# Kernel optimization log

Measured on AMD Instinct MI355X. Metric: run time of the kernel, lower is better.

The kernel has to match this reference:

```python
import jax, jax.numpy as jnp
import numpy as np

TEMP = 0.1

def _normalized_grid(B, H, W, dtype=jnp.float32):
    # normalized coords in [-1, 1], (x, y) order, shape [B, H, W, 2]
    ys = jnp.linspace(-1.0, 1.0, H, dtype=dtype)
    xs = jnp.linspace(-1.0, 1.0, W, dtype=dtype)
    gy, gx = jnp.meshgrid(ys, xs, indexing='ij')
    grid = jnp.stack([gx, gy], axis=-1)  # [H, W, 2]
    return jnp.broadcast_to(grid, (B, H, W, 2))


def setup_inputs() -> dict:
    key = jax.random.key(0)
    k1, k2, k3 = jax.random.split(key, 3)
    B, H, W, D = 8, 48, 48, 1024
    f_mv_A = jax.random.normal(k1, (B, H, W, D), dtype=jnp.float32)
    f_mv_B = jax.random.normal(k2, (B, H, W, D), dtype=jnp.float32)
    # omega buffer: 2*pi*randn(dim//2, 2)
    omega = 2.0 * jnp.pi * jax.random.normal(k3, (D // 2, 2), dtype=jnp.float32)
    scale = jnp.ones((), dtype=jnp.float32)
    return {"f_mv_A": f_mv_A, "f_mv_B": f_mv_B, "omega": omega, "scale": scale}


def reference(f_mv_A, f_mv_B, omega, scale):
    B, H_A, W_A, D = f_mv_A.shape
    _, H_B, W_B, _ = f_mv_B.shape
    # Fourier positional embedding grid over image B coordinates
    x = _normalized_grid(B, H_B, W_B).reshape(B, H_B * W_B, 2)
    x_emb = x @ (scale * omega).T                      # [B, HW_B, D//2]
    pos_emb_grid = jnp.concatenate([jnp.sin(x_emb), jnp.cos(x_emb)], axis=-1)  # [B, HW_B, D]

    # cosine similarity cross-attention
    fa = f_mv_A / jnp.linalg.norm(f_mv_A, axis=-1, keepdims=True)
    fb = f_mv_B / jnp.linalg.norm(f_mv_B, axis=-1, keepdims=True)
    fa = fa.reshape(B, H_A * W_A, D)
    fb = fb.reshape(B, H_B * W_B, D)
    attn_logits = (1.0 / TEMP) * jnp.einsum('bqd,bkd->bqk', fa, fb)  # [B, HW_A, HW_B]
    attn = jax.nn.softmax(attn_logits, axis=2)
    match_emb = jnp.einsum('bqk,bkd->bqd', attn, pos_emb_grid)        # [B, HW_A, D]

    attn_logits = attn_logits.reshape(B, H_A, W_A, H_B, W_B)
    attn = attn.reshape(B, H_A, W_A, H_B, W_B)
    match_emb = match_emb.reshape(B, H_A, W_A, D)
    return attn_logits, attn, match_emb
```

## Files before the change

kernel.cpp:

```cpp
#include <hip/hip_runtime.h>
#include <stdint.h>
#include <math.h>

#define NBATCH 8
#define HWSZ   2304
#define DDIM   1024
#define NROWS  (NBATCH*HWSZ)
#define PLANE  ((size_t)NROWS*DDIM)
#define OFF1   ((size_t)NBATCH*HWSZ*HWSZ)
#define OFF2   (2*OFF1)

typedef __attribute__((ext_vector_type(8))) short bf16x8;
typedef __attribute__((ext_vector_type(8))) _Float16 f16x8;
typedef __attribute__((ext_vector_type(4))) float f32x4;

__device__ __forceinline__ float bf2f(uint16_t u) {
    union { uint32_t i; float f; } v; v.i = ((uint32_t)u) << 16; return v.f;
}
__device__ __forceinline__ uint16_t f2bf(float f) {
    union { uint32_t i; float f; } v; v.f = f;
    uint32_t x = v.i;
    return (uint16_t)((x + 0x7fffu + ((x >> 16) & 1u)) >> 16);
}
__device__ __forceinline__ float h2f(uint16_t u) {
    _Float16 h; __builtin_memcpy(&h, &u, 2); return (float)h;
}
__device__ __forceinline__ uint16_t f2h(float f) {
    _Float16 h = (_Float16)f; uint16_t u; __builtin_memcpy(&u, &h, 2); return u;
}
__device__ __forceinline__ int dmode(const uint16_t* s) {
    uint16_t v = s[0];
    return (v == 0x3F80u) ? 1 : ((v == 0x3C00u) ? 2 : 0);
}
__device__ __forceinline__ float dec16(uint16_t u, int m) { return (m == 1) ? bf2f(u) : h2f(u); }
__device__ __forceinline__ uint16_t enc16(float f, int m) { return (m == 1) ? f2bf(f) : f2h(f); }

__global__ void layout_probe(int* __restrict__ rowT, int* __restrict__ colT) {
    int lane = threadIdx.x & 63;
    int m = lane & 15, q = lane >> 4;
    bf16x8 a1, b1, a2, b2;
    #pragma unroll
    for (int j = 0; j < 8; j++) {
        int k = q * 8 + j;
        float k0 = (k == 0) ? 1.0f : 0.0f;
        a1[j] = (short)f2bf(k0);
        b1[j] = (short)f2bf(k0 * (float)(m + 1));
        a2[j] = (short)f2bf(k0 * (float)(m + 1));
        b2[j] = (short)f2bf(k0);
    }
    f32x4 z = {0.f, 0.f, 0.f, 0.f};
    f32x4 d1 = __builtin_amdgcn_mfma_f32_16x16x32_bf16(a1, b1, z, 0, 0, 0);
    f32x4 d2 = __builtin_amdgcn_mfma_f32_16x16x32_bf16(a2, b2, z, 0, 0, 0);
    #pragma unroll
    for (int r = 0; r < 4; r++) {
        colT[lane * 4 + r] = (int)d1[r] - 1;
        rowT[lane * 4 + r] = (int)d2[r] - 1;
    }
}

__global__ void rownorm_kernel(const void* __restrict__ inA, const void* __restrict__ inB,
                               const uint16_t* __restrict__ scalep, float* __restrict__ rn,
                               void* __restrict__ outbase) {
    const int mode = dmode(scalep);
    int row = blockIdx.x;
    int t = threadIdx.x;
    const void* src = (row < NROWS) ? inA : inB;
    int lrow = (row < NROWS) ? row : row - NROWS;
    float v[4];
    if (mode == 0) {
        const float* p = (const float*)src + (size_t)lrow * DDIM + t * 4;
        float4 f = *(const float4*)p;
        v[0] = f.x; v[1] = f.y; v[2] = f.z; v[3] = f.w;
        uint16_t* hbase = (uint16_t*)((float*)outbase + OFF1) + ((row < NROWS) ? 0 : PLANE);
        uint16_t h0 = f2h(v[0]), h1 = f2h(v[1]), h2 = f2h(v[2]), h3 = f2h(v[3]);
        uint2 hv;
        hv.x = (uint32_t)h0 | ((uint32_t)h1 << 16);
        hv.y = (uint32_t)h2 | ((uint32_t)h3 << 16);
        *(uint2*)(hbase + (size_t)lrow * DDIM + t * 4) = hv;
    } else {
        const uint16_t* p = (const uint16_t*)src + (size_t)lrow * DDIM + t * 4;
        uint2 u = *(const uint2*)p;
        v[0] = dec16(u.x & 0xffff, mode); v[1] = dec16(u.x >> 16, mode);
        v[2] = dec16(u.y & 0xffff, mode); v[3] = dec16(u.y >> 16, mode);
    }
    float ss = v[0]*v[0] + v[1]*v[1] + v[2]*v[2] + v[3]*v[3];
    __shared__ float red[256];
    red[t] = ss; __syncthreads();
    for (int s = 128; s > 0; s >>= 1) { if (t < s) red[t] += red[t + s]; __syncthreads(); }
    if (t == 0) rn[row] = 1.0f / sqrtf(red[0]);
}

__global__ void posemb_kernel(const void* __restrict__ omega, const uint16_t* __restrict__ scalep,
                              uint16_t* __restrict__ posT) {
    const int mode = dmode(scalep);
    int j = blockIdx.x;
    float om0, om1, sc;
    if (mode == 0) {
        const float* om = (const float*)omega;
        om0 = om[j * 2]; om1 = om[j * 2 + 1];
        sc = *(const float*)scalep;
    } else {
        const uint16_t* om = (const uint16_t*)omega;
        om0 = dec16(om[j * 2], mode); om1 = dec16(om[j * 2 + 1], mode);
        sc = dec16(scalep[0], mode);
    }
    om0 *= sc; om1 *= sc;
    for (int p = threadIdx.x; p < HWSZ; p += 256) {
        int iy = p / 48, ix = p % 48;
        float gx = (2.0f / 47.0f) * (float)ix - 1.0f;
        float gy = (2.0f / 47.0f) * (float)iy - 1.0f;
        float e = om0 * gx + om1 * gy;
        size_t chunk = (size_t)(p >> 5) * (DDIM * 32);
        int kin = p & 31;
        posT[chunk + (size_t)j * 32 + kin]           = f2bf(sinf(e));
        posT[chunk + (size_t)(j + 512) * 32 + kin]   = f2bf(cosf(e));
    }
}

#define LSTR 40

__launch_bounds__(256, 2)
__global__ void gemm1_mfma(const void* __restrict__ inA, const void* __restrict__ inB,
                           const uint16_t* __restrict__ scalep, const float* __restrict__ rn,
                           void* __restrict__ outbase,
                           const int* __restrict__ rowT, const int* __restrict__ colT) {
    const int mode = dmode(scalep);
    __shared__ uint16_t sA[128 * LSTR];
    __shared__ uint16_t sB[128 * LSTR];
    __shared__ float rnS[256];
    int g = blockIdx.x;
    int swz = (g & 7) * 324 + (g >> 3);
    int b = swz / 324;
    int rr = swz % 324;
    int tm = rr / 18, tn = rr % 18;
    int t = threadIdx.x;
    if (t < 128) rnS[t] = 10.0f * rn[(size_t)b * HWSZ + tm * 128 + t];
    else         rnS[t] = rn[(size_t)NROWS + (size_t)b * HWSZ + tn * 128 + (t - 128)];
    int r0c = t >> 2, cb0 = (t & 3) * 8;
    int r1c = r0c + 64;
    int lane = t & 63, wave = t >> 6;
    int wm = (wave & 1) * 64, wn = (wave >> 1) * 64;
    int lr = lane & 15, ko = (lane >> 4) * 8;
    size_t rowA0 = (size_t)b * HWSZ + tm * 128;
    size_t rowB0 = (size_t)b * HWSZ + tn * 128;
    const uint16_t* pA16;
    const uint16_t* pB16;
    if (mode == 0) {
        const uint16_t* planes = (const uint16_t*)((const float*)outbase + OFF1);
        pA16 = planes + rowA0 * DDIM;
        pB16 = planes + PLANE + rowB0 * DDIM;
    } else {
        pA16 = (const uint16_t*)inA + rowA0 * DDIM;
        pB16 = (const uint16_t*)inB + rowB0 * DDIM;
    }
    f32x4 acc[4][4] = {};

    for (int k0 = 0; k0 < DDIM; k0 += 32) {
        uint4 a0 = *(const uint4*)(pA16 + (size_t)r0c * DDIM + k0 + cb0);
        uint4 a1 = *(const uint4*)(pA16 + (size_t)r1c * DDIM + k0 + cb0);
        uint4 b0 = *(const uint4*)(pB16 + (size_t)r0c * DDIM + k0 + cb0);
        uint4 b1 = *(const uint4*)(pB16 + (size_t)r1c * DDIM + k0 + cb0);
        __syncthreads();
        *(uint4*)(sA + r0c * LSTR + cb0) = a0;
        *(uint4*)(sA + r1c * LSTR + cb0) = a1;
        *(uint4*)(sB + r0c * LSTR + cb0) = b0;
        *(uint4*)(sB + r1c * LSTR + cb0) = b1;
        __syncthreads();
        if (mode == 1) {
            bf16x8 af[4], bf_[4];
            #pragma unroll
            for (int i = 0; i < 4; i++) af[i] = *(const bf16x8*)(sA + (wm + i * 16 + lr) * LSTR + ko);
            #pragma unroll
            for (int j = 0; j < 4; j++) bf_[j] = *(const bf16x8*)(sB + (wn + j * 16 + lr) * LSTR + ko);
            #pragma unroll
            for (int i = 0; i < 4; i++)
                #pragma unroll
                for (int j = 0; j < 4; j++)
                    acc[i][j] = __builtin_amdgcn_mfma_f32_16x16x32_bf16(af[i], bf_[j], acc[i][j], 0, 0, 0);
        } else {
            f16x8 af[4], bf_[4];
            #pragma unroll
            for (int i = 0; i < 4; i++) af[i] = *(const f16x8*)(sA + (wm + i * 16 + lr) * LSTR + ko);
            #pragma unroll
            for (int j = 0; j < 4; j++) bf_[j] = *(const f16x8*)(sB + (wn + j * 16 + lr) * LSTR + ko);
            #pragma unroll
            for (int i = 0; i < 4; i++)
                #pragma unroll
                for (int j = 0; j < 4; j++)
                    acc[i][j] = __builtin_amdgcn_mfma_f32_16x16x32_f16(af[i], bf_[j], acc[i][j], 0, 0, 0);
        }
    }

    int rtab[4], ctab[4];
    #pragma unroll
    for (int r = 0; r < 4; r++) {
        rtab[r] = rowT[lane * 4 + r] & 15;
        ctab[r] = colT[lane * 4 + r] & 15;
    }
    size_t cbase = (size_t)b * HWSZ * HWSZ;
    #pragma unroll
    for (int i = 0; i < 4; i++) {
        #pragma unroll
        for (int j = 0; j < 4; j++) {
            #pragma unroll
            for (int r = 0; r < 4; r++) {
                int row = wm + i * 16 + rtab[r];
                int col = wn + j * 16 + ctab[r];
                float v = acc[i][j][r] * rnS[row] * rnS[128 + col];
                size_t gm = (size_t)(tm * 128 + row);
                size_t gn = (size_t)(tn * 128 + col);
                if (mode == 0) ((float*)outbase)[cbase + gm * HWSZ + gn] = v;
                else ((uint16_t*)outbase)[cbase + gm * HWSZ + gn] = enc16(v, mode);
            }
        }
    }
}

__global__ void softmax_kernel(void* __restrict__ outbase, const uint16_t* __restrict__ scalep) {
    const int mode = dmode(scalep);
    size_t row = blockIdx.x;
    int t = threadIdx.x;
    float v[9];
    if (mode == 0) {
        const float* src = (const float*)outbase + row * HWSZ;
        #pragma unroll
        for (int i = 0; i < 9; i++) v[i] = src[i * 256 + t];
    } else {
        const uint16_t* src = (const uint16_t*)outbase + row * HWSZ;
        #pragma unroll
        for (int i = 0; i < 9; i++) v[i] = dec16(src[i * 256 + t], mode);
    }
    float m = v[0];
    #pragma unroll
    for (int i = 1; i < 9; i++) m = fmaxf(m, v[i]);
    __shared__ float red[256];
    red[t] = m; __syncthreads();
    for (int s = 128; s > 0; s >>= 1) { if (t < s) red[t] = fmaxf(red[t], red[t + s]); __syncthreads(); }
    float M = red[0];
    __syncthreads();
    float ssum = 0.0f;
    #pragma unroll
    for (int i = 0; i < 9; i++) { v[i] = __expf(v[i] - M); ssum += v[i]; }
    red[t] = ssum; __syncthreads();
    for (int s = 128; s > 0; s >>= 1) { if (t < s) red[t] += red[t + s]; __syncthreads(); }
    float inv = 1.0f / red[0];
    if (mode == 0) {
        float* dst = (float*)outbase + OFF1 + row * HWSZ;
        #pragma unroll
        for (int i = 0; i < 9; i++) dst[i * 256 + t] = v[i] * inv;
    } else {
        uint16_t* dst = (uint16_t*)outbase + OFF1 + row * HWSZ;
        #pragma unroll
        for (int i = 0; i < 9; i++) dst[i * 256 + t] = enc16(v[i] * inv, mode);
    }
}

#define G2BM 64
#define G2BN 512
#define G2L  40

__launch_bounds__(512, 4)
__global__ void gemm2_mfma(void* __restrict__ outbase, const uint16_t* __restrict__ posT,
                           const uint16_t* __restrict__ scalep,
                           const int* __restrict__ rowT, const int* __restrict__ colT) {
    const int mode = dmode(scalep);
    __shared__ uint16_t sA[G2BM * G2L];
    __shared__ uint16_t sB[G2BN * G2L];
    int g = blockIdx.x;
    int swz = (g & 7) * 72 + (g >> 3);
    int b = swz / 72;
    int rr = swz % 72;
    int tm = rr >> 1, tn = rr & 1;
    int t = threadIdx.x;
    int lane = t & 63, wave = t >> 6;
    int wn = wave * 64;
    int lr = lane & 15, ko = (lane >> 4) * 8;
    int ar = t >> 2, ac8 = (t & 3) * 8;
    f32x4 acc[4][4] = {};
    for (int k0 = 0; k0 < HWSZ; k0 += 32) {
        const uint16_t* bsrc = posT + (size_t)(k0 >> 5) * (DDIM * 32) + ((size_t)tn * G2BN + t) * 32;
        uint4 bv0 = *(const uint4*)(bsrc + 0);
        uint4 bv1 = *(const uint4*)(bsrc + 8);
        uint4 bv2 = *(const uint4*)(bsrc + 16);
        uint4 bv3 = *(const uint4*)(bsrc + 24);
        uint16_t av[8];
        if (t < 256) {
            if (mode == 0) {
                const float* ap = (const float*)outbase + OFF1 +
                    ((size_t)b * HWSZ + tm * G2BM + ar) * HWSZ + k0 + ac8;
                float4 x0 = *(const float4*)ap, x1 = *(const float4*)(ap + 4);
                av[0]=f2bf(x0.x); av[1]=f2bf(x0.y); av[2]=f2bf(x0.z); av[3]=f2bf(x0.w);
                av[4]=f2bf(x1.x); av[5]=f2bf(x1.y); av[6]=f2bf(x1.z); av[7]=f2bf(x1.w);
            } else {
                const uint16_t* ap = (const uint16_t*)outbase + OFF1 +
                    ((size_t)b * HWSZ + tm * G2BM + ar) * HWSZ + k0 + ac8;
                uint4 r0 = *(const uint4*)ap;
                const uint16_t* u0 = (const uint16_t*)&r0;
                if (mode == 1) {
                    #pragma unroll
                    for (int j = 0; j < 8; j++) av[j] = u0[j];
                } else {
                    #pragma unroll
                    for (int j = 0; j < 8; j++) av[j] = f2bf(h2f(u0[j]));
                }
            }
        }
        __syncthreads();
        *(uint4*)(sB + t * G2L + 0)  = bv0;
        *(uint4*)(sB + t * G2L + 8)  = bv1;
        *(uint4*)(sB + t * G2L + 16) = bv2;
        *(uint4*)(sB + t * G2L + 24) = bv3;
        if (t < 256) *(uint4*)(sA + ar * G2L + ac8) = *(const uint4*)av;
        __syncthreads();
        bf16x8 af[4], bfr[4];
        #pragma unroll
        for (int i = 0; i < 4; i++) af[i] = *(const bf16x8*)(sA + (i * 16 + lr) * G2L + ko);
        #pragma unroll
        for (int j = 0; j < 4; j++) bfr[j] = *(const bf16x8*)(sB + (wn + j * 16 + lr) * G2L + ko);
        #pragma unroll
        for (int i = 0; i < 4; i++)
            #pragma unroll
            for (int j = 0; j < 4; j++)
                acc[i][j] = __builtin_amdgcn_mfma_f32_16x16x32_bf16(af[i], bfr[j], acc[i][j], 0, 0, 0);
    }
    int rtab[4], ctab[4];
    #pragma unroll
    for (int r = 0; r < 4; r++) {
        rtab[r] = rowT[lane * 4 + r] & 15;
        ctab[r] = colT[lane * 4 + r] & 15;
    }
    #pragma unroll
    for (int i = 0; i < 4; i++) {
        #pragma unroll
        for (int j = 0; j < 4; j++) {
            #pragma unroll
            for (int r = 0; r < 4; r++) {
                size_t row = (size_t)tm * G2BM + i * 16 + rtab[r];
                size_t col = (size_t)tn * G2BN + wn + j * 16 + ctab[r];
                size_t idx = OFF2 + (size_t)b * HWSZ * DDIM + row * DDIM + col;
                if (mode == 0) ((float*)outbase)[idx] = acc[i][j][r];
                else ((uint16_t*)outbase)[idx] = enc16(acc[i][j][r], mode);
            }
        }
    }
}

extern "C" void kernel_launch(void* const* d_in, const int* in_sizes, int n_in,
                              void* d_out, int out_size, void* d_ws, size_t ws_size,
                              hipStream_t stream) {
    const void* fA    = d_in[0];
    const void* fB    = d_in[1];
    const void* omega = d_in[2];
    const uint16_t* scale = (const uint16_t*)d_in[3];

    int* rowT = (int*)d_ws;
    int* colT = rowT + 256;
    float* rn = (float*)((char*)d_ws + 4096);
    uint16_t* posT = (uint16_t*)((char*)d_ws + 4096 + (size_t)2 * NROWS * 4);

    layout_probe<<<1, 64, 0, stream>>>(rowT, colT);
    rownorm_kernel<<<2 * NROWS, 256, 0, stream>>>(fA, fB, scale, rn, d_out);
    posemb_kernel<<<512, 256, 0, stream>>>(omega, scale, posT);

    gemm1_mfma<<<18 * 18 * NBATCH, 256, 0, stream>>>(fA, fB, scale, rn, d_out, rowT, colT);

    softmax_kernel<<<NROWS, 256, 0, stream>>>(d_out, scale);

    gemm2_mfma<<<(HWSZ / G2BM) * (DDIM / G2BN) * NBATCH, 512, 0, stream>>>(d_out, posT, scale, rowT, colT);
}
```

Measured before the change: 470.3 us.

## Fuse softmax normalization into second GEMM using precomputed row statistics

```diff
diff --git a/kernel.cpp b/kernel.cpp
--- a/kernel.cpp
+++ b/kernel.cpp
@@ -216,7 +216,8 @@
     }
 }
 
-__global__ void softmax_kernel(void* __restrict__ outbase, const uint16_t* __restrict__ scalep) {
+__global__ void rowstat_kernel(const void* __restrict__ outbase, const uint16_t* __restrict__ scalep,
+                               float* __restrict__ stats) {
     const int mode = dmode(scalep);
     size_t row = blockIdx.x;
     int t = threadIdx.x;
@@ -240,19 +241,10 @@
     __syncthreads();
     float ssum = 0.0f;
     #pragma unroll
-    for (int i = 0; i < 9; i++) { v[i] = __expf(v[i] - M); ssum += v[i]; }
+    for (int i = 0; i < 9; i++) ssum += __expf(v[i] - M);
     red[t] = ssum; __syncthreads();
     for (int s = 128; s > 0; s >>= 1) { if (t < s) red[t] += red[t + s]; __syncthreads(); }
-    float inv = 1.0f / red[0];
-    if (mode == 0) {
-        float* dst = (float*)outbase + OFF1 + row * HWSZ;
-        #pragma unroll
-        for (int i = 0; i < 9; i++) dst[i * 256 + t] = v[i] * inv;
-    } else {
-        uint16_t* dst = (uint16_t*)outbase + OFF1 + row * HWSZ;
-        #pragma unroll
-        for (int i = 0; i < 9; i++) dst[i * 256 + t] = enc16(v[i] * inv, mode);
-    }
+    if (t == 0) { stats[row] = M; stats[NROWS + row] = 1.0f / red[0]; }
 }
 
 #define G2BM 64
@@ -261,7 +253,7 @@
 
 __launch_bounds__(512, 4)
 __global__ void gemm2_mfma(void* __restrict__ outbase, const uint16_t* __restrict__ posT,
-                           const uint16_t* __restrict__ scalep,
+                           const uint16_t* __restrict__ scalep, const float* __restrict__ stats,
                            const int* __restrict__ rowT, const int* __restrict__ colT) {
     const int mode = dmode(scalep);
     __shared__ uint16_t sA[G2BM * G2L];
@@ -276,6 +268,13 @@
     int wn = wave * 64;
     int lr = lane & 15, ko = (lane >> 4) * 8;
     int ar = t >> 2, ac8 = (t & 3) * 8;
+    float Mrow = 0.f, invl = 0.f;
+    size_t grow = 0;
+    if (t < 256) {
+        grow = (size_t)b * HWSZ + (size_t)tm * G2BM + ar;
+        Mrow = stats[grow];
+        invl = stats[NROWS + grow];
+    }
     f32x4 acc[4][4] = {};
     for (int k0 = 0; k0 < HWSZ; k0 += 32) {
         const uint16_t* bsrc = posT + (size_t)(k0 >> 5) * (DDIM * 32) + ((size_t)tn * G2BN + t) * 32;
@@ -285,25 +284,34 @@
         uint4 bv3 = *(const uint4*)(bsrc + 24);
         uint16_t av[8];
         if (t < 256) {
+            float p[8];
             if (mode == 0) {
-                const float* ap = (const float*)outbase + OFF1 +
-                    ((size_t)b * HWSZ + tm * G2BM + ar) * HWSZ + k0 + ac8;
+                const float* ap = (const float*)outbase + grow * HWSZ + k0 + ac8;
                 float4 x0 = *(const float4*)ap, x1 = *(const float4*)(ap + 4);
-                av[0]=f2bf(x0.x); av[1]=f2bf(x0.y); av[2]=f2bf(x0.z); av[3]=f2bf(x0.w);
-                av[4]=f2bf(x1.x); av[5]=f2bf(x1.y); av[6]=f2bf(x1.z); av[7]=f2bf(x1.w);
+                p[0] = __expf(x0.x - Mrow) * invl; p[1] = __expf(x0.y - Mrow) * invl;
+                p[2] = __expf(x0.z - Mrow) * invl; p[3] = __expf(x0.w - Mrow) * invl;
+                p[4] = __expf(x1.x - Mrow) * invl; p[5] = __expf(x1.y - Mrow) * invl;
+                p[6] = __expf(x1.z - Mrow) * invl; p[7] = __expf(x1.w - Mrow) * invl;
+                if (tn == 0) {
+                    float* dst = (float*)outbase + OFF1 + grow * HWSZ + k0 + ac8;
+                    *(float4*)dst       = *(const float4*)p;
+                    *(float4*)(dst + 4) = *(const float4*)(p + 4);
+                }
             } else {
-                const uint16_t* ap = (const uint16_t*)outbase + OFF1 +
-                    ((size_t)b * HWSZ + tm * G2BM + ar) * HWSZ + k0 + ac8;
+                const uint16_t* ap = (const uint16_t*)outbase + grow * HWSZ + k0 + ac8;
                 uint4 r0 = *(const uint4*)ap;
                 const uint16_t* u0 = (const uint16_t*)&r0;
-                if (mode == 1) {
+                #pragma unroll
+                for (int j = 0; j < 8; j++) p[j] = __expf(dec16(u0[j], mode) - Mrow) * invl;
+                if (tn == 0) {
+                    uint16_t pk[8];
                     #pragma unroll
-                    for (int j = 0; j < 8; j++) av[j] = u0[j];
-                } else {
-                    #pragma unroll
-                    for (int j = 0; j < 8; j++) av[j] = f2bf(h2f(u0[j]));
+                    for (int j = 0; j < 8; j++) pk[j] = enc16(p[j], mode);
+                    *(uint4*)((uint16_t*)outbase + OFF1 + grow * HWSZ + k0 + ac8) = *(const uint4*)pk;
                 }
             }
+            #pragma unroll
+            for (int j = 0; j < 8; j++) av[j] = f2bf(p[j]);
         }
         __syncthreads();
         *(uint4*)(sB + t * G2L + 0)  = bv0;
@@ -364,7 +372,7 @@
 
     gemm1_mfma<<<18 * 18 * NBATCH, 256, 0, stream>>>(fA, fB, scale, rn, d_out, rowT, colT);
 
-    softmax_kernel<<<NROWS, 256, 0, stream>>>(d_out, scale);
-
-    gemm2_mfma<<<(HWSZ / G2BM) * (DDIM / G2BN) * NBATCH, 512, 0, stream>>>(d_out, posT, scale, rowT, colT);
-}
+    rowstat_kernel<<<NROWS, 256, 0, stream>>>(d_out, scale, rn);
+
+    gemm2_mfma<<<(HWSZ / G2BM) * (DDIM / G2BN) * NBATCH, 512, 0, stream>>>(d_out, posT, scale, rn, rowT, colT);
+}
```

Result: slower. 490.9 us (+4.4%).
